# Performance work log

Measured on AMD Instinct MI355X. Metric: run time of the kernel, lower is better.

The kernel has to match this reference:

```python
import jax, jax.numpy as jnp
import numpy as np

# MemoryMLP(dim=64, depth=3, expansion_factor=4) wrapped in ResidualNorm (lucidrains titans-pytorch)
B, N, DIM, HID = 4, 256, 64, 256
DTOT = DIM * HID + HID * HID + HID * DIM + DIM  # 98368 flattened param width
EPS = 1.1920929e-07  # fp32 machine eps, matches torch.nn.RMSNorm(eps=None)
MAX_GRAD_NORM = 5.0
DECAY = 0.9999  # decay_factor = 0.9999 hardcoded in store_memories


def _rmsnorm(x, w):
    return x * jax.lax.rsqrt(jnp.mean(x * x, axis=-1, keepdims=True) + EPS) * w


def _xavier(key, fan_in, fan_out):
    lim = (6.0 / (fan_in + fan_out)) ** 0.5
    return jax.random.uniform(key, (fan_in, fan_out), jnp.float32, -lim, lim)


def setup_inputs() -> dict:
    key = jax.random.key(0)
    k0, k1, k2, k3 = jax.random.split(key, 4)
    return {
        "seq": jax.random.normal(k0, (3, B, N, DIM), jnp.float32),
        "w0": _xavier(k1, DIM, HID),
        "w1": _xavier(k2, HID, HID),
        "w2": _xavier(k3, HID, DIM),
        "norm_w": jnp.ones((DIM,), jnp.float32),        # ResidualNorm RMSNorm weight
        "store_norm_w": jnp.ones((DIM,), jnp.float32),  # store_norm RMSNorm weight
    }


def _token_loss(params, x, y):
    # functional_call(ResidualNorm(MemoryMLP)) + default_loss_fn for one token
    w0, w1, w2, nw = params
    h = x @ w0                                     # first layer: no activation before matmul
    h = jax.nn.gelu(h, approximate=False) @ w1     # torch F.gelu default = exact erf
    h = jax.nn.gelu(h, approximate=False) @ w2
    pred = _rmsnorm(h, nw) + x                     # ResidualNorm: norm(model(x)) + x
    return jnp.mean((pred - y) ** 2)               # (pred - target).pow(2).mean(-1), .sum() is identity for 1 token


def _softclamp_grad(g):
    # softclamp_grad_norm: per-token per-param-tensor norm, softclamped to MAX_GRAD_NORM
    b, n = g.shape[0], g.shape[1]
    flat = g.reshape(b, n, -1)
    nrm = jnp.linalg.norm(flat, axis=-1, keepdims=True)
    half = MAX_GRAD_NORM / 2.0
    clamped = jnp.tanh(nrm / half) * half + half
    return flat * (clamped / nrm)


def _forward(seq, w0, w1, w2, norm_w, store_norm_w):
    # seq: (3, B, N, DIM) = (retrieved, key, value); store_norm applied to key/value only
    kv = _rmsnorm(seq[1:], store_norm_w)
    keys, values = kv[0], kv[1]  # (B, N, DIM)

    # per-sample grads: vmap(grad) over batch and token dims (weights are broadcast-shared)
    grad_fn = jax.grad(_token_loss)
    per_tok = jax.vmap(jax.vmap(grad_fn, in_axes=(None, 0, 0)), in_axes=(None, 0, 0))
    g0, g1, g2, gn = per_tok((w0, w1, w2, norm_w), keys, values)

    # surprises = -clamped grads, flattened+concatenated to one (B, N, DTOT) scan input
    surprise = -jnp.concatenate([_softclamp_grad(g) for g in (g0, g1, g2, gn)], axis=-1)

    # prev = init weights (past_state starts as current weights), prepended with gate=1
    prev = jnp.concatenate([w.reshape(-1) for w in (w0, w1, w2, norm_w)])  # (DTOT,)
    prev = jnp.broadcast_to(prev[None, None, :], (B, 1, DTOT))
    inputs = jnp.concatenate([prev, surprise], axis=1)  # (B, N+1, DTOT)

    gate = jnp.float32(1.0 - DECAY)  # assoc_scan gates = 1 - decay_factor = 1e-4
    gates = jnp.concatenate(
        [jnp.ones((B, 1, 1), jnp.float32), jnp.full((B, N, 1), gate, jnp.float32)], axis=1
    )

    def bin_op(a, b):
        ga, xa = a
        gb, xb = b
        return ga * gb, gb * xa + xb  # out_t = gate_t * out_{t-1} + in_t

    _, out = jax.lax.associative_scan(bin_op, (gates, inputs), axis=1)
    return out  # (B, N+1, DTOT): remove_prev=False keeps the prepended prev state


def reference(seq, w0, w1, w2, norm_w, store_norm_w):
    return _forward(seq, w0, w1, w2, norm_w, store_norm_w)
```

## Files before the change

kernel.cpp:

```cpp
#include <hip/hip_runtime.h>
#include <math.h>

#define DIMV 64
#define HIDV 256
#define BB 4
#define NN 256
#define DTOT 98368
#define STRIDE_B ((size_t)257 * DTOT)
#define EPSV 1.1920929e-07f
#define PREV_BLOCKS ((DTOT + 255) / 256)

__device__ __forceinline__ float wave_sum(float v) {
#pragma unroll
    for (int o = 32; o > 0; o >>= 1) v += __shfl_down(v, o, 64);
    return v;
}

__device__ __forceinline__ float block_sum(float v, float* red) {
    int tid = threadIdx.x;
    float s = wave_sum(v);
    __syncthreads();
    if ((tid & 63) == 0) red[tid >> 6] = s;
    __syncthreads();
    return red[0] + red[1] + red[2] + red[3];
}

__device__ __forceinline__ void block_sum2(float v0, float v1, float* red,
                                           float& r0, float& r1) {
    int tid = threadIdx.x;
    float s0 = wave_sum(v0), s1 = wave_sum(v1);
    __syncthreads();
    if ((tid & 63) == 0) { int w = tid >> 6; red[w] = s0; red[4 + w] = s1; }
    __syncthreads();
    r0 = red[0] + red[1] + red[2] + red[3];
    r1 = red[4] + red[5] + red[6] + red[7];
}

__device__ __forceinline__ void block_sum3(float v0, float v1, float v2, float* red,
                                           float& r0, float& r1, float& r2) {
    int tid = threadIdx.x;
    float s0 = wave_sum(v0), s1 = wave_sum(v1), s2 = wave_sum(v2);
    __syncthreads();
    if ((tid & 63) == 0) {
        int w = tid >> 6;
        red[w] = s0; red[4 + w] = s1; red[8 + w] = s2;
    }
    __syncthreads();
    r0 = red[0] + red[1] + red[2] + red[3];
    r1 = red[4] + red[5] + red[6] + red[7];
    r2 = red[8] + red[9] + red[10] + red[11];
}

__device__ __forceinline__ float geluf(float z) {
    return 0.5f * z * (1.0f + erff(z * 0.70710678118654752f));
}
__device__ __forceinline__ float dgeluf(float z) {
    float cdf = 0.5f * (1.0f + erff(z * 0.70710678118654752f));
    float pdf = 0.3989422804014327f * expf(-0.5f * z * z);
    return cdf + z * pdf;
}

__global__ __launch_bounds__(256) void token_grad_kernel(
    const float* __restrict__ seq, const float* __restrict__ w0,
    const float* __restrict__ w1, const float* __restrict__ w2,
    const float* __restrict__ norm_w, const float* __restrict__ snw,
    const float* __restrict__ w1b,
    const float* __restrict__ w2b,
    int tw,
    float* __restrict__ out)
{
    __shared__ __align__(16) float sx[DIMV], sy[DIMV], nw_s[DIMV];
    __shared__ __align__(16) float h0s[HIDV], a0s[HIDV], h1s[HIDV], a1s[HIDV];
    __shared__ __align__(16) float h2s[DIMV], dh2s[DIMV], dh1s[HIDV], dh0s[HIDV], gns[DIMV];
    __shared__ float red[12];
    __shared__ __align__(16) float part[256];

    const int tid = threadIdx.x;
    const int blk = blockIdx.x;
    const int b = blk >> 8;
    const int t = blk & 255;

    float xr = 0.f, yr = 0.f, sw = 0.f;
    if (tid < DIMV) {
        size_t kofs = ((size_t)(1 * BB + b) * NN + t) * DIMV + tid;
        size_t vofs = ((size_t)(2 * BB + b) * NN + t) * DIMV + tid;
        xr = seq[kofs];
        yr = seq[vofs];
        sw = snw[tid];
        nw_s[tid] = norm_w[tid];
    }
    float sxx, syy, sxs;
    block_sum3(tid < DIMV ? xr * xr : 0.f,
               tid < DIMV ? yr * yr : 0.f,
               tid < DIMV ? xr * xr * sw * sw : 0.f, red, sxx, syy, sxs);
    float invx = rsqrtf(sxx * (1.0f / 64.0f) + EPSV);
    float invy = rsqrtf(syy * (1.0f / 64.0f) + EPSV);
    if (tid < DIMV) {
        sx[tid] = xr * invx * sw;
        sy[tid] = yr * invy * sw;
    }
    float x_nrm2 = sxs * invx * invx;
    __syncthreads();

    float acc0 = 0.f;
#pragma unroll 8
    for (int i = 0; i < DIMV; i++) acc0 = fmaf(sx[i], w0[i * HIDV + tid], acc0);
    h0s[tid] = acc0;
    float a0v = geluf(acc0);
    a0s[tid] = a0v;
    __syncthreads();

    float acc1 = 0.f;
#pragma unroll 8
    for (int k = 0; k < HIDV; k++) acc1 = fmaf(a0s[k], w1[k * HIDV + tid], acc1);
    h1s[tid] = acc1;
    float a1v = geluf(acc1);
    a1s[tid] = a1v;
    __syncthreads();

    {
        int p = tid >> 6, j = tid & 63;
        float a = 0.f;
#pragma unroll 8
        for (int k = p * 64; k < p * 64 + 64; k++) a = fmaf(a1s[k], w2[k * DIMV + j], a);
        part[tid] = a;
    }
    __syncthreads();
    if (tid < DIMV) h2s[tid] = part[tid] + part[tid + 64] + part[tid + 128] + part[tid + 192];
    __syncthreads();

    float h2v = (tid < DIMV) ? h2s[tid] : 0.f;
    float sh2 = block_sum(h2v * h2v, red);
    float inv = rsqrtf(sh2 * (1.0f / 64.0f) + EPSV);

    float dpredv = 0.f, gnv = 0.f;
    if (tid < DIMV) {
        float pred = h2v * inv * nw_s[tid] + sx[tid];
        dpredv = (2.0f / 64.0f) * (pred - sy[tid]);
        gnv = dpredv * h2v * inv;
        gns[tid] = gnv;
    }
    float S, gn2;
    block_sum2(tid < DIMV ? dpredv * nw_s[tid] * h2v : 0.f, gnv * gnv, red, S, gn2);

    float dh2v = 0.f;
    if (tid < DIMV) {
        dh2v = dpredv * inv * nw_s[tid] - (inv * inv * inv * (1.0f / 64.0f)) * h2v * S;
        dh2s[tid] = dh2v;
    }
    float dh2_2, a1_2;
    block_sum2(dh2v * dh2v, a1v * a1v, red, dh2_2, a1_2);

    float da1 = 0.f;
    if (tw) {
#pragma unroll 8
        for (int j = 0; j < DIMV; j++) da1 = fmaf(w2b[j * HIDV + tid], dh2s[j], da1);
    } else {
#pragma unroll 8
        for (int j = 0; j < DIMV; j++) da1 = fmaf(w2b[tid * DIMV + j], dh2s[j], da1);
    }
    float dh1v = da1 * dgeluf(h1s[tid]);
    dh1s[tid] = dh1v;
    float dh1_2, a0_2;
    block_sum2(dh1v * dh1v, a0v * a0v, red, dh1_2, a0_2);

    float da0 = 0.f;
    if (tw) {
#pragma unroll 8
        for (int l = 0; l < HIDV; l++) da0 = fmaf(w1b[l * HIDV + tid], dh1s[l], da0);
    } else {
#pragma unroll 8
        for (int l = 0; l < HIDV; l++) da0 = fmaf(w1b[tid * HIDV + l], dh1s[l], da0);
    }
    float dh0v = da0 * dgeluf(h0s[tid]);
    dh0s[tid] = dh0v;
    float dh0_2 = block_sum(dh0v * dh0v, red);

    float n0 = sqrtf(x_nrm2 * dh0_2);
    float n1 = sqrtf(a0_2 * dh1_2);
    float n2 = sqrtf(a1_2 * dh2_2);
    float nn = sqrtf(gn2);
    float s0 = -(tanhf(n0 * 0.4f) * 2.5f + 2.5f) / n0;
    float s1 = -(tanhf(n1 * 0.4f) * 2.5f + 2.5f) / n1;
    float s2 = -(tanhf(n2 * 0.4f) * 2.5f + 2.5f) / n2;
    float sn = -(tanhf(nn * 0.4f) * 2.5f + 2.5f) / nn;

    size_t obase = ((size_t)b * 257 + (size_t)(t + 1)) * DTOT;

    {
        float4* o0 = (float4*)(out + obase);
#pragma unroll
        for (int it = 0; it < 16; it++) {
            int e = (it * 256 + tid) * 4;
            int i = e >> 8, c = e & 255;
            float f = s0 * sx[i];
            float4 v = make_float4(f * dh0s[c], f * dh0s[c + 1], f * dh0s[c + 2], f * dh0s[c + 3]);
            o0[it * 256 + tid] = v;
        }
    }
    {
        float4* o1 = (float4*)(out + obase + 16384);
#pragma unroll 4
        for (int it = 0; it < 64; it++) {
            int e = (it * 256 + tid) * 4;
            int k = e >> 8, c = e & 255;
            float f = s1 * a0s[k];
            float4 v = make_float4(f * dh1s[c], f * dh1s[c + 1], f * dh1s[c + 2], f * dh1s[c + 3]);
            o1[it * 256 + tid] = v;
        }
    }
    {
        float4* o2 = (float4*)(out + obase + 81920);
#pragma unroll
        for (int it = 0; it < 16; it++) {
            int e = (it * 256 + tid) * 4;
            int k = e >> 6, c = e & 63;
            float f = s2 * a1s[k];
            float4 v = make_float4(f * dh2s[c], f * dh2s[c + 1], f * dh2s[c + 2], f * dh2s[c + 3]);
            o2[it * 256 + tid] = v;
        }
    }
    if (tid < 16) {
        int c = tid * 4;
        float4 v = make_float4(sn * gns[c], sn * gns[c + 1], sn * gns[c + 2], sn * gns[c + 3]);
        ((float4*)(out + obase + 98304))[tid] = v;
    }
}

__global__ __launch_bounds__(256) void setup_kernel(
    const float* __restrict__ w0, const float* __restrict__ w1,
    const float* __restrict__ w2, const float* __restrict__ nw,
    float* __restrict__ out, float* __restrict__ w1t, float* __restrict__ w2t)
{
    int blk = blockIdx.x;
    if (blk < PREV_BLOCKS) {
        int idx = blk * 256 + threadIdx.x;
        if (idx >= DTOT) return;
        float v;
        if (idx < 16384) v = w0[idx];
        else if (idx < 81920) v = w1[idx - 16384];
        else if (idx < 98304) v = w2[idx - 81920];
        else v = nw[idx - 98304];
#pragma unroll
        for (int b = 0; b < BB; b++) out[(size_t)b * STRIDE_B + idx] = v;
        return;
    }
    __shared__ float tile[64][65];
    int t2 = blk - PREV_BLOCKS;
    const float* src; float* dst; int C, tr, tc;
    if (t2 < 16) { src = w1; dst = w1t; C = 256; tr = t2 >> 2; tc = t2 & 3; }
    else         { src = w2; dst = w2t; C = 64;  tr = t2 - 16; tc = 0; }

    int c  = threadIdx.x & 63;
    int r0 = (threadIdx.x >> 6) * 16;
#pragma unroll
    for (int i = 0; i < 16; i++) {
        int r = r0 + i;
        tile[r][c] = src[(size_t)(tr * 64 + r) * C + (tc * 64 + c)];
    }
    __syncthreads();
    int rr  = threadIdx.x & 63;
    int cc0 = (threadIdx.x >> 6) * 16;
#pragma unroll
    for (int i = 0; i < 16; i++) {
        int cc = cc0 + i;
        dst[(size_t)(tc * 64 + cc) * 256 + (tr * 64 + rr)] = tile[rr][cc];
    }
}

extern "C" void kernel_launch(void* const* d_in, const int* in_sizes, int n_in,
                              void* d_out, int out_size, void* d_ws, size_t ws_size,
                              hipStream_t stream) {
    const float* seq = (const float*)d_in[0];
    const float* w0  = (const float*)d_in[1];
    const float* w1  = (const float*)d_in[2];
    const float* w2  = (const float*)d_in[3];
    const float* nw  = (const float*)d_in[4];
    const float* snw = (const float*)d_in[5];
    float* out = (float*)d_out;

    float* w1t = (float*)d_ws;
    float* w2t = w1t ? w1t + 65536 : nullptr;
    const size_t need = (size_t)(65536 + 16384) * sizeof(float);
    int tw = (d_ws != nullptr && ws_size >= need) ? 1 : 0;

    hipLaunchKernelGGL(setup_kernel, dim3(tw ? PREV_BLOCKS + 20 : PREV_BLOCKS), dim3(256),
                       0, stream, w0, w1, w2, nw, out, w1t, w2t);
    hipLaunchKernelGGL(token_grad_kernel, dim3(BB * NN), dim3(256), 0, stream,
                       seq, w0, w1, w2, nw, snw,
                       tw ? w1t : w1, tw ? w2t : w2, tw, out);
}
```

Measured before the change: 442.2 us.

## Vectorize matvecs with float4 split-K partials and interleave gradient stores with backward

Each per-token matvec (forward and transposed backward) now loads float4 weight rows, with each wave handling a slice of the K dimension; partial sums are reduced through a larger shared buffer. The outer-product gradient stores for w2, norm and w1 are moved earlier, right after their scale factors are known, so the large global writes can overlap the remaining backward matvecs. Pre-activation shared buffers are replaced by register values. The cost is extra shared memory and extra syncs, which may lower occupancy.

```diff
diff --git a/kernel.cpp b/kernel.cpp
--- a/kernel.cpp
+++ b/kernel.cpp
@@ -70,15 +70,18 @@
     float* __restrict__ out)
 {
     __shared__ __align__(16) float sx[DIMV], sy[DIMV], nw_s[DIMV];
-    __shared__ __align__(16) float h0s[HIDV], a0s[HIDV], h1s[HIDV], a1s[HIDV];
-    __shared__ __align__(16) float h2s[DIMV], dh2s[DIMV], dh1s[HIDV], dh0s[HIDV], gns[DIMV];
+    __shared__ __align__(16) float a0s[HIDV], a1s[HIDV];
+    __shared__ __align__(16) float dh2s[DIMV], dh1s[HIDV], dh0s[HIDV], gns[DIMV];
     __shared__ float red[12];
-    __shared__ __align__(16) float part[256];
+    __shared__ __align__(16) float part[1024];
+    float4* part4 = (float4*)part;
 
     const int tid = threadIdx.x;
     const int blk = blockIdx.x;
     const int b = blk >> 8;
     const int t = blk & 255;
+    const int q  = tid >> 6;
+    const int c4 = tid & 63;
 
     float xr = 0.f, yr = 0.f, sw = 0.f;
     if (tid < DIMV) {
@@ -102,34 +105,64 @@
     float x_nrm2 = sxs * invx * invx;
     __syncthreads();
 
-    float acc0 = 0.f;
-#pragma unroll 8
-    for (int i = 0; i < DIMV; i++) acc0 = fmaf(sx[i], w0[i * HIDV + tid], acc0);
-    h0s[tid] = acc0;
+    {
+        const float4* w04 = (const float4*)w0;
+        float4 p = make_float4(0.f, 0.f, 0.f, 0.f);
+#pragma unroll
+        for (int kk = 0; kk < 16; kk++) {
+            int k = q * 16 + kk;
+            float xv = sx[k];
+            float4 wv = w04[k * 64 + c4];
+            p.x = fmaf(xv, wv.x, p.x); p.y = fmaf(xv, wv.y, p.y);
+            p.z = fmaf(xv, wv.z, p.z); p.w = fmaf(xv, wv.w, p.w);
+        }
+        part4[q * 64 + c4] = p;
+    }
+    __syncthreads();
+    float acc0 = part[tid] + part[256 + tid] + part[512 + tid] + part[768 + tid];
     float a0v = geluf(acc0);
     a0s[tid] = a0v;
     __syncthreads();
 
-    float acc1 = 0.f;
+    {
+        const float4* w14 = (const float4*)w1;
+        float4 p = make_float4(0.f, 0.f, 0.f, 0.f);
 #pragma unroll 8
-    for (int k = 0; k < HIDV; k++) acc1 = fmaf(a0s[k], w1[k * HIDV + tid], acc1);
-    h1s[tid] = acc1;
+        for (int kk = 0; kk < 64; kk++) {
+            int k = q * 64 + kk;
+            float av = a0s[k];
+            float4 wv = w14[k * 64 + c4];
+            p.x = fmaf(av, wv.x, p.x); p.y = fmaf(av, wv.y, p.y);
+            p.z = fmaf(av, wv.z, p.z); p.w = fmaf(av, wv.w, p.w);
+        }
+        part4[q * 64 + c4] = p;
+    }
+    __syncthreads();
+    float acc1 = part[tid] + part[256 + tid] + part[512 + tid] + part[768 + tid];
     float a1v = geluf(acc1);
     a1s[tid] = a1v;
     __syncthreads();
 
     {
-        int p = tid >> 6, j = tid & 63;
-        float a = 0.f;
-#pragma unroll 8
-        for (int k = p * 64; k < p * 64 + 64; k++) a = fmaf(a1s[k], w2[k * DIMV + j], a);
-        part[tid] = a;
-    }
-    __syncthreads();
-    if (tid < DIMV) h2s[tid] = part[tid] + part[tid + 64] + part[tid + 128] + part[tid + 192];
-    __syncthreads();
-
-    float h2v = (tid < DIMV) ? h2s[tid] : 0.f;
+        const float4* w24 = (const float4*)w2;
+        int p16 = tid >> 4, c4h = tid & 15;
+        float4 p = make_float4(0.f, 0.f, 0.f, 0.f);
+#pragma unroll
+        for (int kk = 0; kk < 16; kk++) {
+            int k = p16 * 16 + kk;
+            float av = a1s[k];
+            float4 wv = w24[k * 16 + c4h];
+            p.x = fmaf(av, wv.x, p.x); p.y = fmaf(av, wv.y, p.y);
+            p.z = fmaf(av, wv.z, p.z); p.w = fmaf(av, wv.w, p.w);
+        }
+        part4[p16 * 16 + c4h] = p;
+    }
+    __syncthreads();
+    float h2v = 0.f;
+    if (tid < DIMV) {
+#pragma unroll
+        for (int p16 = 0; p16 < 16; p16++) h2v += part[p16 * 64 + tid];
+    }
     float sh2 = block_sum(h2v * h2v, red);
     float inv = rsqrtf(sh2 * (1.0f / 64.0f) + EPSV);
 
@@ -151,79 +184,105 @@
     float dh2_2, a1_2;
     block_sum2(dh2v * dh2v, a1v * a1v, red, dh2_2, a1_2);
 
+    float n2 = sqrtf(a1_2 * dh2_2);
+    float nn = sqrtf(gn2);
+    float s2 = -(tanhf(n2 * 0.4f) * 2.5f + 2.5f) / n2;
+    float sn = -(tanhf(nn * 0.4f) * 2.5f + 2.5f) / nn;
+
+    size_t obase = ((size_t)b * 257 + (size_t)(t + 1)) * DTOT;
+
+    {
+        float4* o2 = (float4*)(out + obase + 81920);
+#pragma unroll
+        for (int it = 0; it < 16; it++) {
+            int k = it * 16 + (tid >> 4);
+            int c = (tid * 4) & 63;
+            float f = s2 * a1s[k];
+            float4 d = *(const float4*)&dh2s[c];
+            o2[it * 256 + tid] = make_float4(f * d.x, f * d.y, f * d.z, f * d.w);
+        }
+    }
+    if (tid < 16) {
+        int c = tid * 4;
+        float4 g = *(const float4*)&gns[c];
+        ((float4*)(out + obase + 98304))[tid] = make_float4(sn * g.x, sn * g.y, sn * g.z, sn * g.w);
+    }
+
     float da1 = 0.f;
     if (tw) {
-#pragma unroll 8
-        for (int j = 0; j < DIMV; j++) da1 = fmaf(w2b[j * HIDV + tid], dh2s[j], da1);
+        const float4* w2t4 = (const float4*)w2b;
+        float4 p = make_float4(0.f, 0.f, 0.f, 0.f);
+#pragma unroll
+        for (int jj = 0; jj < 16; jj++) {
+            int j = q * 16 + jj;
+            float dv = dh2s[j];
+            float4 wv = w2t4[j * 64 + c4];
+            p.x = fmaf(dv, wv.x, p.x); p.y = fmaf(dv, wv.y, p.y);
+            p.z = fmaf(dv, wv.z, p.z); p.w = fmaf(dv, wv.w, p.w);
+        }
+        part4[q * 64 + c4] = p;
+        __syncthreads();
+        da1 = part[tid] + part[256 + tid] + part[512 + tid] + part[768 + tid];
     } else {
 #pragma unroll 8
         for (int j = 0; j < DIMV; j++) da1 = fmaf(w2b[tid * DIMV + j], dh2s[j], da1);
     }
-    float dh1v = da1 * dgeluf(h1s[tid]);
+    float dh1v = da1 * dgeluf(acc1);
     dh1s[tid] = dh1v;
     float dh1_2, a0_2;
     block_sum2(dh1v * dh1v, a0v * a0v, red, dh1_2, a0_2);
 
+    float n1 = sqrtf(a0_2 * dh1_2);
+    float s1 = -(tanhf(n1 * 0.4f) * 2.5f + 2.5f) / n1;
+
+    {
+        float4* o1 = (float4*)(out + obase + 16384);
+#pragma unroll 4
+        for (int it = 0; it < 64; it++) {
+            int k = it * 4 + (tid >> 6);
+            int c = (tid * 4) & 255;
+            float f = s1 * a0s[k];
+            float4 d = *(const float4*)&dh1s[c];
+            o1[it * 256 + tid] = make_float4(f * d.x, f * d.y, f * d.z, f * d.w);
+        }
+    }
+
     float da0 = 0.f;
     if (tw) {
+        const float4* w1t4 = (const float4*)w1b;
+        float4 p = make_float4(0.f, 0.f, 0.f, 0.f);
 #pragma unroll 8
-        for (int l = 0; l < HIDV; l++) da0 = fmaf(w1b[l * HIDV + tid], dh1s[l], da0);
+        for (int ll = 0; ll < 64; ll++) {
+            int l = q * 64 + ll;
+            float dv = dh1s[l];
+            float4 wv = w1t4[l * 64 + c4];
+            p.x = fmaf(dv, wv.x, p.x); p.y = fmaf(dv, wv.y, p.y);
+            p.z = fmaf(dv, wv.z, p.z); p.w = fmaf(dv, wv.w, p.w);
+        }
+        part4[q * 64 + c4] = p;
+        __syncthreads();
+        da0 = part[tid] + part[256 + tid] + part[512 + tid] + part[768 + tid];
     } else {
 #pragma unroll 8
         for (int l = 0; l < HIDV; l++) da0 = fmaf(w1b[tid * HIDV + l], dh1s[l], da0);
     }
-    float dh0v = da0 * dgeluf(h0s[tid]);
+    float dh0v = da0 * dgeluf(acc0);
     dh0s[tid] = dh0v;
     float dh0_2 = block_sum(dh0v * dh0v, red);
 
     float n0 = sqrtf(x_nrm2 * dh0_2);
-    float n1 = sqrtf(a0_2 * dh1_2);
-    float n2 = sqrtf(a1_2 * dh2_2);
-    float nn = sqrtf(gn2);
     float s0 = -(tanhf(n0 * 0.4f) * 2.5f + 2.5f) / n0;
-    float s1 = -(tanhf(n1 * 0.4f) * 2.5f + 2.5f) / n1;
-    float s2 = -(tanhf(n2 * 0.4f) * 2.5f + 2.5f) / n2;
-    float sn = -(tanhf(nn * 0.4f) * 2.5f + 2.5f) / nn;
-
-    size_t obase = ((size_t)b * 257 + (size_t)(t + 1)) * DTOT;
 
     {
         float4* o0 = (float4*)(out + obase);
 #pragma unroll
         for (int it = 0; it < 16; it++) {
-            int e = (it * 256 + tid) * 4;
-            int i = e >> 8, c = e & 255;
+            int i = it * 4 + (tid >> 6);
+            int c = (tid * 4) & 255;
             float f = s0 * sx[i];
-            float4 v = make_float4(f * dh0s[c], f * dh0s[c + 1], f * dh0s[c + 2], f * dh0s[c + 3]);
-            o0[it * 256 + tid] = v;
-        }
-    }
-    {
-        float4* o1 = (float4*)(out + obase + 16384);
-#pragma unroll 4
-        for (int it = 0; it < 64; it++) {
-            int e = (it * 256 + tid) * 4;
-            int k = e >> 8, c = e & 255;
-            float f = s1 * a0s[k];
-            float4 v = make_float4(f * dh1s[c], f * dh1s[c + 1], f * dh1s[c + 2], f * dh1s[c + 3]);
-            o1[it * 256 + tid] = v;
-        }
-    }
-    {
-        float4* o2 = (float4*)(out + obase + 81920);
-#pragma unroll
-        for (int it = 0; it < 16; it++) {
-            int e = (it * 256 + tid) * 4;
-            int k = e >> 6, c = e & 63;
-            float f = s2 * a1s[k];
-            float4 v = make_float4(f * dh2s[c], f * dh2s[c + 1], f * dh2s[c + 2], f * dh2s[c + 3]);
-            o2[it * 256 + tid] = v;
-        }
-    }
-    if (tid < 16) {
-        int c = tid * 4;
-        float4 v = make_float4(sn * gns[c], sn * gns[c + 1], sn * gns[c + 2], sn * gns[c + 3]);
-        ((float4*)(out + obase + 98304))[tid] = v;
+            float4 d = *(const float4*)&dh0s[c];
+            o0[it * 256 + tid] = make_float4(f * d.x, f * d.y, f * d.z, f * d.w);
+        }
     }
 }
 
```

Result: faster. 423.0 us (-4.3%).
